# Performance work log

Hardware: AMD Instinct MI355X
Metric: run time of the kernel (lower is better)

Reference implementation:

```python
import jax, jax.numpy as jnp
import numpy as np

SEQ = 4096
EMB = 1024
OUT = 1024


def setup_inputs() -> dict:
    key = jax.random.key(0)
    k_x, k_q, k_k, k_v = jax.random.split(key, 4)
    scale = 1.0 / np.sqrt(EMB)
    inputs = jax.random.normal(k_x, (SEQ, EMB), dtype=jnp.float32)
    # torch Linear weight is (out_features, in_features); y = x @ W.T
    W_Q = jax.random.normal(k_q, (OUT, EMB), dtype=jnp.float32) * scale
    W_K = jax.random.normal(k_k, (OUT, EMB), dtype=jnp.float32) * scale
    W_V = jax.random.normal(k_v, (OUT, EMB), dtype=jnp.float32) * scale
    return {"inputs": inputs, "W_Q": W_Q, "W_K": W_K, "W_V": W_V}


def reference(inputs, W_Q, W_K, W_V):
    # projections: (S, E) @ (E, D) -> (S, D)
    q = inputs @ W_Q.T
    k = inputs @ W_K.T
    v = inputs @ W_V.T
    d_k = k.shape[-1]
    scores = (q @ k.T) / jnp.sqrt(jnp.asarray(d_k, dtype=q.dtype))  # (S, S)
    weights = jax.nn.softmax(scores, axis=-1)
    return weights @ v  # (S, D)
```

## Files before the change

kernel.cpp:

```cpp
#include <hip/hip_runtime.h>

typedef __bf16 bf16;
typedef __bf16 bf16x4 __attribute__((ext_vector_type(4)));
typedef __bf16 bf16x8 __attribute__((ext_vector_type(8)));
typedef float f32x4 __attribute__((ext_vector_type(4)));

#define SEQ 4096
#define EMB 1024

__device__ __forceinline__ void async_copy16(void* lds, const void* g) {
    __builtin_amdgcn_global_load_lds(
        (const __attribute__((address_space(1))) unsigned int*)g,
        (__attribute__((address_space(3))) unsigned int*)lds,
        16, 0, 0);
}

__global__ __launch_bounds__(256) void prep_all(const float* __restrict__ x,
                                                const float* __restrict__ wq,
                                                const float* __restrict__ wk,
                                                const float* __restrict__ wv,
                                                bf16* __restrict__ xb,
                                                bf16* __restrict__ wqk,
                                                bf16* __restrict__ wvb,
                                                float* __restrict__ rowsum)
{
    const int u = blockIdx.x * 256 + threadIdx.x;
    const float* src;
    bf16* dst;
    int off;
    if (u < 1048576)      { src = x;  dst = xb;               off = u; }
    else if (u < 1310720) { src = wq; dst = wqk;              off = u - 1048576; }
    else if (u < 1572864) { src = wk; dst = wqk + EMB * EMB;  off = u - 1310720; }
    else if (u < 1835008) { src = wv; dst = wvb;              off = u - 1572864; }
    else {
        *(float4*)(rowsum + (size_t)(u - 1835008) * 4) = float4{0.f, 0.f, 0.f, 0.f};
        return;
    }
    float4 f = *(const float4*)(src + (size_t)off * 4);
    bf16x4 v = { (bf16)f.x, (bf16)f.y, (bf16)f.z, (bf16)f.w };
    *(bf16x4*)(dst + (size_t)off * 4) = v;
}

template<bool RSUM>
__device__ __forceinline__ void tile_step(int t, int NT,
                                          const bf16* __restrict__ Ab,
                                          const bf16* __restrict__ Bb,
                                          int lda, int ldb,
                                          bf16* __restrict__ As,
                                          bf16* __restrict__ Bs,
                                          bf16* __restrict__ AsD,
                                          bf16* __restrict__ BsD,
                                          int wr, int wc, int fr, int pc,
                                          bf16x8 (&afA)[4], bf16x8 (&afB)[4],
                                          bf16x8 (&bgC)[4], bf16x8 (&bgN)[4],
                                          f32x4 (&acc)[8][4], float (&rsum)[8],
                                          bool rs_active)
{
    if (t + 2 < NT) {
        const int b2 = ((t + 2) & 3) * 8192;
        async_copy16(AsD + b2,        Ab + (t + 2) * 32);
        async_copy16(AsD + b2 + 4096, Ab + (t + 2) * 32 + (size_t)128 * lda);
    }
    {
        const bf16* At = As + (t & 3) * 8192 + (wr * 128 + 64 + fr) * 32 + pc;
#pragma unroll
        for (int mf = 0; mf < 4; mf++)
            afB[mf] = *(const bf16x8*)(At + (mf * 16) * 32);
    }
    asm volatile("s_waitcnt lgkmcnt(4)" ::: "memory");
    __builtin_amdgcn_sched_barrier(0);
    __builtin_amdgcn_s_setprio(1);
#pragma unroll
    for (int nj = 0; nj < 4; nj++)
#pragma unroll
        for (int mf = 0; mf < 4; mf++)
            acc[mf][nj] = __builtin_amdgcn_mfma_f32_16x16x32_bf16(afA[mf], bgC[nj], acc[mf][nj], 0, 0, 0);
    __builtin_amdgcn_s_setprio(0);
    if (RSUM && rs_active) {
#pragma unroll
        for (int mf = 0; mf < 4; mf++)
#pragma unroll
            for (int e = 0; e < 8; e++) rsum[mf] += (float)afA[mf][e];
    }

    if (t < NT - 1) {
        if (t + 2 < NT) {
            asm volatile("s_waitcnt vmcnt(2)" ::: "memory");
        } else {
            asm volatile("s_waitcnt vmcnt(0)" ::: "memory");
        }
        __builtin_amdgcn_s_barrier();
        if (t + 2 < NT) {
            const int b2 = ((t + 2) & 3) * 8192;
            async_copy16(BsD + b2,        Bb + (t + 2) * 32);
            async_copy16(BsD + b2 + 4096, Bb + (t + 2) * 32 + (size_t)128 * ldb);
        }
        {
            const int b1 = ((t + 1) & 3) * 8192;
            const bf16* At = As + b1 + (wr * 128 + fr) * 32 + pc;
            const bf16* Bt = Bs + b1 + (wc * 64 + fr) * 32 + pc;
#pragma unroll
            for (int mf = 0; mf < 4; mf++)
                afA[mf] = *(const bf16x8*)(At + (mf * 16) * 32);
#pragma unroll
            for (int nj = 0; nj < 4; nj++)
                bgN[nj] = *(const bf16x8*)(Bt + (nj * 16) * 32);
        }
        asm volatile("s_waitcnt lgkmcnt(8)" ::: "memory");
        __builtin_amdgcn_sched_barrier(0);
    } else {
        asm volatile("s_waitcnt lgkmcnt(0)" ::: "memory");
        __builtin_amdgcn_sched_barrier(0);
    }
    __builtin_amdgcn_s_setprio(1);
#pragma unroll
    for (int nj = 0; nj < 4; nj++)
#pragma unroll
        for (int mf = 0; mf < 4; mf++)
            acc[4 + mf][nj] = __builtin_amdgcn_mfma_f32_16x16x32_bf16(afB[mf], bgC[nj], acc[4 + mf][nj], 0, 0, 0);
    __builtin_amdgcn_s_setprio(0);
    if (RSUM && rs_active) {
#pragma unroll
        for (int mf = 0; mf < 4; mf++)
#pragma unroll
            for (int e = 0; e < 8; e++) rsum[4 + mf] += (float)afB[mf][e];
    }
}

template<bool RSUM>
__device__ __forceinline__ void gemm_core256(const bf16* __restrict__ A,
                                             const bf16* __restrict__ B,
                                             int lda, int ldb, long koff,
                                             int m0, int n0,
                                             bf16* __restrict__ As,
                                             bf16* __restrict__ Bs,
                                             f32x4 (&acc)[8][4], float (&rsum)[8],
                                             bool rs_active)
{
    const int tid  = threadIdx.x;
    const int lane = tid & 63;
    const int wave = tid >> 6;
    const int wr = wave >> 2;
    const int wc = wave & 3;
    const int srow = tid >> 2;
    const int spc  = tid & 3;
    const int sl   = (spc - ((srow >> 1) & 3)) & 3;
    const int fr = lane & 15;
    const int q  = lane >> 4;
    const int pc = ((q + ((fr >> 1) & 3)) & 3) * 8;
    const int NT = 32;

#pragma unroll
    for (int i = 0; i < 8; i++)
#pragma unroll
        for (int j = 0; j < 4; j++) acc[i][j] = {0.f, 0.f, 0.f, 0.f};
    if (RSUM)
#pragma unroll
        for (int i = 0; i < 8; i++) rsum[i] = 0.f;

    const bf16* Ab = A + (size_t)(m0 + srow) * lda + koff + sl * 8;
    const bf16* Bb = B + (size_t)(n0 + srow) * ldb + koff + sl * 8;
    bf16* AsD = As + srow * 32 + spc * 8;
    bf16* BsD = Bs + srow * 32 + spc * 8;

#pragma unroll
    for (int tt = 0; tt < 2; tt++) {
        async_copy16(AsD + tt * 8192,        Ab + tt * 32);
        async_copy16(AsD + tt * 8192 + 4096, Ab + tt * 32 + (size_t)128 * lda);
        async_copy16(BsD + tt * 8192,        Bb + tt * 32);
        async_copy16(BsD + tt * 8192 + 4096, Bb + tt * 32 + (size_t)128 * ldb);
    }
    asm volatile("s_waitcnt vmcnt(4)" ::: "memory");
    __builtin_amdgcn_s_barrier();

    bf16x8 afA[4], afB[4], bg0[4], bg1[4];
    {
        const bf16* At = As + (wr * 128 + fr) * 32 + pc;
        const bf16* Bt = Bs + (wc * 64 + fr) * 32 + pc;
#pragma unroll
        for (int mf = 0; mf < 4; mf++)
            afA[mf] = *(const bf16x8*)(At + (mf * 16) * 32);
#pragma unroll
        for (int nj = 0; nj < 4; nj++)
            bg0[nj] = *(const bf16x8*)(Bt + (nj * 16) * 32);
    }

    for (int t = 0; t < NT; t += 2) {
        tile_step<RSUM>(t,     NT, Ab, Bb, lda, ldb, As, Bs, AsD, BsD,
                        wr, wc, fr, pc, afA, afB, bg0, bg1, acc, rsum, rs_active);
        tile_step<RSUM>(t + 1, NT, Ab, Bb, lda, ldb, As, Bs, AsD, BsD,
                        wr, wc, fr, pc, afA, afB, bg1, bg0, acc, rsum, rs_active);
    }
}

__global__ __launch_bounds__(512, 1) void gemm_proj(const bf16* __restrict__ xb,
                                                    const bf16* __restrict__ wqk,
                                                    const bf16* __restrict__ wvb,
                                                    bf16* __restrict__ QK,
                                                    bf16* __restrict__ VT)
{
    __shared__ __align__(16) bf16 As[4][8192];
    __shared__ __align__(16) bf16 Bs[4][8192];

    const bf16 *A, *B;
    bf16* C;
    int ldc, m0, n0;
    if (blockIdx.y < 8) {
        A = xb; B = wqk; C = QK; ldc = 2048;
        m0 = blockIdx.x * 256; n0 = blockIdx.y * 256;
    } else {
        const int id = blockIdx.x + (blockIdx.y - 8) * 16;
        A = wvb; B = xb; C = VT; ldc = 4096;
        m0 = (id & 3) * 256; n0 = (id >> 2) * 256;
    }

    f32x4 acc[8][4];
    float rs[8];
    gemm_core256<false>(A, B, 1024, 1024, 0, m0, n0, &As[0][0], &Bs[0][0], acc, rs, false);

    const int lane = threadIdx.x & 63;
    const int wave = threadIdx.x >> 6;
    const int cm = m0 + (wave >> 2) * 128 + ((lane >> 4) << 2);
    const int cn = n0 + (wave & 3) * 64 + (lane & 15);
#pragma unroll
    for (int i = 0; i < 8; i++)
#pragma unroll
        for (int j = 0; j < 4; j++)
#pragma unroll
            for (int r = 0; r < 4; r++)
                C[(size_t)(cm + i * 16 + r) * ldc + (cn + j * 16)] = (bf16)acc[i][j][r];
}

__global__ __launch_bounds__(512, 1) void gemm_exp(const bf16* __restrict__ QK,
                                                   bf16* __restrict__ E)
{
    __shared__ __align__(16) bf16 As[4][8192];
    __shared__ __align__(16) bf16 Bs[4][8192];

    const int m0 = blockIdx.x * 256;
    const int n0 = blockIdx.y * 256;
    f32x4 acc[8][4];
    float rs[8];
    gemm_core256<false>(QK, QK + 1024, 2048, 2048, 0, m0, n0, &As[0][0], &Bs[0][0], acc, rs, false);

    const int lane = threadIdx.x & 63;
    const int wave = threadIdx.x >> 6;
    const int cm = m0 + (wave >> 2) * 128 + ((lane >> 4) << 2);
    const int cn = n0 + (wave & 3) * 64 + (lane & 15);
#pragma unroll
    for (int i = 0; i < 8; i++)
#pragma unroll
        for (int j = 0; j < 4; j++)
#pragma unroll
            for (int r = 0; r < 4; r++)
                E[(size_t)(cm + i * 16 + r) * 4096 + (cn + j * 16)] =
                    (bf16)__expf(acc[i][j][r] * 0.03125f);
}

__global__ __launch_bounds__(512, 1) void gemm_pv(const bf16* __restrict__ E,
                                                  const bf16* __restrict__ VT,
                                                  float* __restrict__ out,
                                                  float* __restrict__ p1,
                                                  float* __restrict__ rowsum)
{
    __shared__ __align__(16) bf16 As[4][8192];
    __shared__ __align__(16) bf16 Bs[4][8192];

    const int m0 = blockIdx.x * 256;
    const int n0 = blockIdx.y * 256;
    const long koff = (long)blockIdx.z * 1024;
    const bool rs_active = (blockIdx.y == 0) && (((threadIdx.x >> 6) & 3) == 0);

    f32x4 acc[8][4];
    float rs[8];
    gemm_core256<true>(E, VT, 4096, 4096, koff, m0, n0, &As[0][0], &Bs[0][0], acc, rs, rs_active);

    const int lane = threadIdx.x & 63;
    const int wave = threadIdx.x >> 6;
    if (rs_active) {
#pragma unroll
        for (int i = 0; i < 8; i++) {
            rs[i] += __shfl_xor(rs[i], 16);
            rs[i] += __shfl_xor(rs[i], 32);
        }
        if (lane < 16) {
            const int rbase = m0 + (wave >> 2) * 128;
#pragma unroll
            for (int i = 0; i < 8; i++)
                unsafeAtomicAdd(&rowsum[rbase + i * 16 + lane], rs[i]);
        }
    }

    float* C = (blockIdx.z == 0) ? out : p1 + (size_t)(blockIdx.z - 1) * SEQ * 1024;
    const int cm = m0 + (wave >> 2) * 128 + ((lane >> 4) << 2);
    const int cn = n0 + (wave & 3) * 64 + (lane & 15);
#pragma unroll
    for (int i = 0; i < 8; i++)
#pragma unroll
        for (int j = 0; j < 4; j++)
#pragma unroll
            for (int r = 0; r < 4; r++)
                C[(size_t)(cm + i * 16 + r) * 1024 + (cn + j * 16)] = acc[i][j][r];
}

__global__ __launch_bounds__(256) void reduce_norm(float* __restrict__ out,
                                                   const float* __restrict__ p1,
                                                   const float* __restrict__ p2,
                                                   const float* __restrict__ p3,
                                                   const float* __restrict__ rowsum)
{
    const int m = blockIdx.x;
    const float inv = 1.f / rowsum[m];
    const size_t off = (size_t)m * 1024 + threadIdx.x * 4;
    float4 a = *(const float4*)(out + off);
    float4 b = *(const float4*)(p1 + off);
    float4 c = *(const float4*)(p2 + off);
    float4 d = *(const float4*)(p3 + off);
    float4 o;
    o.x = (a.x + b.x + c.x + d.x) * inv;
    o.y = (a.y + b.y + c.y + d.y) * inv;
    o.z = (a.z + b.z + c.z + d.z) * inv;
    o.w = (a.w + b.w + c.w + d.w) * inv;
    *(float4*)(out + off) = o;
}

extern "C" void kernel_launch(void* const* d_in, const int* in_sizes, int n_in,
                              void* d_out, int out_size, void* d_ws, size_t ws_size,
                              hipStream_t stream)
{
    const float* x  = (const float*)d_in[0];
    const float* wq = (const float*)d_in[1];
    const float* wk = (const float*)d_in[2];
    const float* wv = (const float*)d_in[3];
    float* out = (float*)d_out;

    char* ws = (char*)d_ws;
    const size_t MB = 1024 * 1024;
    bf16*  E   = (bf16*)(ws);
    float* p1  = (float*)(ws + 32 * MB);
    float* p2  = (float*)(ws + 48 * MB);
    float* p3  = (float*)(ws + 64 * MB);
    bf16*  xb  = (bf16*)(ws + 32 * MB);
    bf16*  wqk = (bf16*)(ws + 40 * MB);
    bf16*  wvb = (bf16*)(ws + 44 * MB);
    bf16*  QK  = (bf16*)(ws + 64 * MB);
    bf16*  VT  = (bf16*)(ws + 80 * MB);
    float* rsm = (float*)(ws + 88 * MB);

    prep_all<<<dim3(7172), dim3(256), 0, stream>>>(x, wq, wk, wv, xb, wqk, wvb, rsm);
    gemm_proj<<<dim3(16, 12), dim3(512), 0, stream>>>(xb, wqk, wvb, QK, VT);
    gemm_exp<<<dim3(16, 16), dim3(512), 0, stream>>>(QK, E);
    gemm_pv<<<dim3(16, 4, 4), dim3(512), 0, stream>>>(E, VT, out, p1, rsm);
    reduce_norm<<<dim3(4096), dim3(256), 0, stream>>>(out, p1, p2, p3, rsm);
}
```

Before: 203.8 us.

## Deepen async LDS prefetch to three stages and remap blocks per XCD

```diff
diff --git a/kernel.cpp b/kernel.cpp
--- a/kernel.cpp
+++ b/kernel.cpp
@@ -56,11 +56,6 @@
                                           f32x4 (&acc)[8][4], float (&rsum)[8],
                                           bool rs_active)
 {
-    if (t + 2 < NT) {
-        const int b2 = ((t + 2) & 3) * 8192;
-        async_copy16(AsD + b2,        Ab + (t + 2) * 32);
-        async_copy16(AsD + b2 + 4096, Ab + (t + 2) * 32 + (size_t)128 * lda);
-    }
     {
         const bf16* At = As + (t & 3) * 8192 + (wr * 128 + 64 + fr) * 32 + pc;
 #pragma unroll
@@ -84,16 +79,19 @@
     }
 
     if (t < NT - 1) {
+        asm volatile("s_waitcnt lgkmcnt(0)" ::: "memory");
         if (t + 2 < NT) {
-            asm volatile("s_waitcnt vmcnt(2)" ::: "memory");
+            asm volatile("s_waitcnt vmcnt(4)" ::: "memory");
         } else {
             asm volatile("s_waitcnt vmcnt(0)" ::: "memory");
         }
         __builtin_amdgcn_s_barrier();
-        if (t + 2 < NT) {
-            const int b2 = ((t + 2) & 3) * 8192;
-            async_copy16(BsD + b2,        Bb + (t + 2) * 32);
-            async_copy16(BsD + b2 + 4096, Bb + (t + 2) * 32 + (size_t)128 * ldb);
+        if (t + 3 < NT) {
+            const int b3 = ((t + 3) & 3) * 8192;
+            async_copy16(AsD + b3,        Ab + (t + 3) * 32);
+            async_copy16(AsD + b3 + 4096, Ab + (t + 3) * 32 + (size_t)128 * lda);
+            async_copy16(BsD + b3,        Bb + (t + 3) * 32);
+            async_copy16(BsD + b3 + 4096, Bb + (t + 3) * 32 + (size_t)128 * ldb);
         }
         {
             const int b1 = ((t + 1) & 3) * 8192;
@@ -106,7 +104,6 @@
             for (int nj = 0; nj < 4; nj++)
                 bgN[nj] = *(const bf16x8*)(Bt + (nj * 16) * 32);
         }
-        asm volatile("s_waitcnt lgkmcnt(8)" ::: "memory");
         __builtin_amdgcn_sched_barrier(0);
     } else {
         asm volatile("s_waitcnt lgkmcnt(0)" ::: "memory");
@@ -164,13 +161,13 @@
     bf16* BsD = Bs + srow * 32 + spc * 8;
 
 #pragma unroll
-    for (int tt = 0; tt < 2; tt++) {
+    for (int tt = 0; tt < 3; tt++) {
         async_copy16(AsD + tt * 8192,        Ab + tt * 32);
         async_copy16(AsD + tt * 8192 + 4096, Ab + tt * 32 + (size_t)128 * lda);
         async_copy16(BsD + tt * 8192,        Bb + tt * 32);
         async_copy16(BsD + tt * 8192 + 4096, Bb + tt * 32 + (size_t)128 * ldb);
     }
-    asm volatile("s_waitcnt vmcnt(4)" ::: "memory");
+    asm volatile("s_waitcnt vmcnt(8)" ::: "memory");
     __builtin_amdgcn_s_barrier();
 
     bf16x8 afA[4], afB[4], bg0[4], bg1[4];
@@ -202,14 +199,20 @@
     __shared__ __align__(16) bf16 As[4][8192];
     __shared__ __align__(16) bf16 Bs[4][8192];
 
+    const int hw  = blockIdx.x + 16 * blockIdx.y;
+    const int xcd = hw & 7;
+    const int s   = hw >> 3;
+    const int bx  = ((xcd & 1) << 3) | (s & 7);
+    const int byy = (xcd >> 1) * 3 + (s >> 3);
+
     const bf16 *A, *B;
     bf16* C;
     int ldc, m0, n0;
-    if (blockIdx.y < 8) {
+    if (byy < 8) {
         A = xb; B = wqk; C = QK; ldc = 2048;
-        m0 = blockIdx.x * 256; n0 = blockIdx.y * 256;
+        m0 = bx * 256; n0 = byy * 256;
     } else {
-        const int id = blockIdx.x + (blockIdx.y - 8) * 16;
+        const int id = bx + (byy - 8) * 16;
         A = wvb; B = xb; C = VT; ldc = 4096;
         m0 = (id & 3) * 256; n0 = (id >> 2) * 256;
     }
@@ -237,8 +240,14 @@
     __shared__ __align__(16) bf16 As[4][8192];
     __shared__ __align__(16) bf16 Bs[4][8192];
 
-    const int m0 = blockIdx.x * 256;
-    const int n0 = blockIdx.y * 256;
+    const int hw  = blockIdx.x + 16 * blockIdx.y;
+    const int xcd = hw & 7;
+    const int s   = hw >> 3;
+    const int bx  = ((xcd & 1) << 3) | (s & 7);
+    const int by  = ((xcd >> 1) << 2) | (s >> 3);
+
+    const int m0 = bx * 256;
+    const int n0 = by * 256;
     f32x4 acc[8][4];
     float rs[8];
     gemm_core256<false>(QK, QK + 1024, 2048, 2048, 0, m0, n0, &As[0][0], &Bs[0][0], acc, rs, false);
@@ -266,10 +275,17 @@
     __shared__ __align__(16) bf16 As[4][8192];
     __shared__ __align__(16) bf16 Bs[4][8192];
 
-    const int m0 = blockIdx.x * 256;
-    const int n0 = blockIdx.y * 256;
-    const long koff = (long)blockIdx.z * 1024;
-    const bool rs_active = (blockIdx.y == 0) && (((threadIdx.x >> 6) & 3) == 0);
+    const int hw  = blockIdx.x + 16 * blockIdx.y + 64 * blockIdx.z;
+    const int xcd = hw & 7;
+    const int s   = hw >> 3;
+    const int bx  = ((xcd & 1) << 3) | (s & 7);
+    const int by  = s >> 3;
+    const int bz  = xcd >> 1;
+
+    const int m0 = bx * 256;
+    const int n0 = by * 256;
+    const long koff = (long)bz * 1024;
+    const bool rs_active = (by == 0) && (((threadIdx.x >> 6) & 3) == 0);
 
     f32x4 acc[8][4];
     float rs[8];
@@ -291,7 +307,7 @@
         }
     }
 
-    float* C = (blockIdx.z == 0) ? out : p1 + (size_t)(blockIdx.z - 1) * SEQ * 1024;
+    float* C = (bz == 0) ? out : p1 + (size_t)(bz - 1) * SEQ * 1024;
     const int cm = m0 + (wave >> 2) * 128 + ((lane >> 4) << 2);
     const int cn = n0 + (wave & 3) * 64 + (lane & 15);
 #pragma unroll
```

Result: slower. 233.1 us (+14.4%).
